# Performance work log

Hardware: AMD Instinct MI355X
Metric: run time of the kernel (lower is better)

Reference implementation:

```python
import jax, jax.numpy as jnp
import numpy as np

B, Q, K, H = 8, 512, 512, 1024
NH, HD = 16, 64
MAX_REL = 512  # max_relative_positions


def setup_inputs() -> dict:
    key = jax.random.key(0)
    ks = jax.random.split(key, 16)
    s = 1.0 / np.sqrt(H)
    inp = {
        "query": jax.random.normal(ks[0], (B, Q, H), jnp.float32),
        "key": jax.random.normal(ks[1], (B, K, H), jnp.float32),
        "value": jax.random.normal(ks[2], (B, K, H), jnp.float32),
        "key_padding_mask": jax.random.randint(ks[3], (B, K), 0, 2, jnp.int32),
        "Wq": jax.random.normal(ks[4], (H, H), jnp.float32) * s,
        "bq": jnp.zeros((H,), jnp.float32),
        "Wk": jax.random.normal(ks[5], (H, H), jnp.float32) * s,
        "bk": jnp.zeros((H,), jnp.float32),
        "Wv": jax.random.normal(ks[6], (H, H), jnp.float32) * s,
        "bv": jnp.zeros((H,), jnp.float32),
        "Wo": jax.random.normal(ks[7], (H, H), jnp.float32) * s,
        "bo": jnp.zeros((H,), jnp.float32),
        "rel_table": jax.random.normal(ks[8], (2 * MAX_REL - 1, NH), jnp.float32) * 0.02,
        "local_bias": jax.random.normal(ks[9], (512, 512), jnp.float32) * 0.1,
        "log_scale": jnp.zeros((1,), jnp.float32),
        "attention_bias": jnp.zeros((1,), jnp.float32),
    }
    return inp


def reference(query, key, value, key_padding_mask, Wq, bq, Wk, bk, Wv, bv, Wo, bo,
              rel_table, local_bias, log_scale, attention_bias):
    # projections -> [B, NH, len, HD]
    q = (query @ Wq + bq).reshape(B, Q, NH, HD).transpose(0, 2, 1, 3)
    k = (key @ Wk + bk).reshape(B, K, NH, HD).transpose(0, 2, 1, 3)
    v = (value @ Wv + bv).reshape(B, K, NH, HD).transpose(0, 2, 1, 3)

    scores = jnp.einsum('bhqd,bhkd->bhqk', q, k) / jnp.sqrt(jnp.float32(HD))

    # relative position bias
    rel = jnp.arange(Q)[:, None] - jnp.arange(K)[None, :]
    bucket = jnp.clip(rel, -(MAX_REL - 1), MAX_REL - 1) + (MAX_REL - 1)
    rel_bias = rel_table[bucket]            # [Q, K, NH]
    scores = scores + rel_bias.transpose(2, 0, 1)[None]  # [1, NH, Q, K]

    # local bias (Q,K <= 512)
    scores = scores + local_bias[:Q, :K][None, None] * 0.05

    scale = jnp.clip(jnp.exp(log_scale), 1.0, 4.0)
    scores = scores * scale + attention_bias

    pad = (key_padding_mask == 0)[:, None, None, :]  # [B,1,1,K]
    scores = jnp.where(pad, -jnp.inf, scores)
    # clamp AFTER masking: -inf -> -50 (padded keys get tiny but nonzero weight)
    scores = jnp.clip(scores, -50.0, 50.0)

    attn = jax.nn.softmax(scores, axis=-1)
    out = jnp.einsum('bhqk,bhkd->bhqd', attn, v)
    out = out.transpose(0, 2, 1, 3).reshape(B, Q, H)
    out = out @ Wo + bo
    return out, attn
```

## Files before the change

### kernel.cpp

```cpp
#include <hip/hip_runtime.h>

#define B_ 8
#define LQ 512
#define LK 512
#define HDIM 1024
#define NH_ 16
#define HD_ 64

typedef unsigned short u16;
typedef __attribute__((ext_vector_type(4))) float f32x4;
typedef __attribute__((ext_vector_type(4))) int i32x4;
typedef __attribute__((ext_vector_type(8))) __bf16 bf16x8;

static __device__ __forceinline__ u16 f2bf(float f) {
    union { float f; unsigned u; } v; v.f = f;
    unsigned u = v.u;
    return (u16)((u + 0x7fffu + ((u >> 16) & 1u)) >> 16);
}

static __device__ __forceinline__ float bf2f(u16 u) {
    union { unsigned u; float f; } v; v.u = ((unsigned)u) << 16;
    return v.f;
}

static __device__ __forceinline__ void gload_lds16(const u16* g, u16* l) {
    __builtin_amdgcn_global_load_lds((const __attribute__((address_space(1))) unsigned*)g,
                                     (__attribute__((address_space(3))) unsigned*)l, 16, 0, 0);
}

__global__ __launch_bounds__(256) void xcast_kernel(
    const float* __restrict__ x0, const float* __restrict__ x1, const float* __restrict__ x2,
    u16* __restrict__ o0, u16* __restrict__ o1, u16* __restrict__ o2)
{
    const float* X; u16* O;
    switch (blockIdx.z) { case 0: X = x0; O = o0; break; case 1: X = x1; O = o1; break;
                          default: X = x2; O = o2; }
    int i = blockIdx.x * 256 + threadIdx.x;
    f32x4 v = ((const f32x4*)X)[i];
    union { u16 u[4]; unsigned long long ull; } p;
    p.u[0] = f2bf(v[0]); p.u[1] = f2bf(v[1]); p.u[2] = f2bf(v[2]); p.u[3] = f2bf(v[3]);
    ((unsigned long long*)O)[i] = p.ull;
}

__global__ void wcast_kernel(const float* __restrict__ w0, const float* __restrict__ w1,
                             const float* __restrict__ w2, const float* __restrict__ w3,
                             u16* __restrict__ o0, u16* __restrict__ o1,
                             u16* __restrict__ o2, u16* __restrict__ o3) {
    const float* W; u16* O;
    switch (blockIdx.z) { case 0: W = w0; O = o0; break; case 1: W = w1; O = o1; break;
                          case 2: W = w2; O = o2; break; default: W = w3; O = o3; }
    __shared__ float t[32][33];
    int tx = threadIdx.x, ty = threadIdx.y;
    int n0 = blockIdx.x * 32, k0 = blockIdx.y * 32;
#pragma unroll
    for (int i = 0; i < 4; i++) {
        int k = ty * 4 + i;
        t[k][tx] = W[(k0 + k) * HDIM + n0 + tx];
    }
    __syncthreads();
#pragma unroll
    for (int i = 0; i < 4; i++) {
        int n = ty * 4 + i;
        O[(n0 + n) * HDIM + k0 + tx] = f2bf(t[tx][n]);
    }
}

__global__ __launch_bounds__(256) void biasprep_kernel(
    const float* __restrict__ rel_table, const float* __restrict__ local_bias,
    const float* __restrict__ log_scale, const float* __restrict__ att_bias,
    u16* __restrict__ Tb)
{
    int idx = blockIdx.x * 256 + threadIdx.x;
    int base = idx * 8;
    int h = base >> 18;
    int rem = base & 262143;
    int qi = rem >> 9, ki0 = rem & 511;
    float scale = fminf(fmaxf(__expf(log_scale[0]), 1.0f), 4.0f);
    float ab = att_bias[0];
    union { u16 u[8]; i32x4 v; } o;
#pragma unroll
    for (int t = 0; t < 8; t++) {
        int ki = ki0 + t;
        float r = rel_table[(qi - ki + 511) * NH_ + h];
        float lb = local_bias[qi * 512 + ki];
        o.u[t] = f2bf((r + lb * 0.05f) * scale + ab);
    }
    *(i32x4*)&Tb[base] = o.v;
}

__global__ __launch_bounds__(256) void proj2_kernel(
    const u16* __restrict__ x0, const u16* __restrict__ x1, const u16* __restrict__ x2,
    const u16* __restrict__ wt0, const u16* __restrict__ wt1, const u16* __restrict__ wt2,
    const float* __restrict__ bi0, const float* __restrict__ bi1, const float* __restrict__ bi2,
    u16* __restrict__ ot0, u16* __restrict__ ot1, u16* __restrict__ ot2)
{
    __shared__ u16 As[128 * 64];
    __shared__ u16 Bs[128 * 64];
    int bid = blockIdx.x;
    int swz = (bid & 7) * 96 + (bid >> 3);
    int z = swz >> 8, rem = swz & 255;
    int Mb = (rem >> 3) * 128, Nb = (rem & 7) * 128;
    const u16* X; const u16* WT; const float* bias; u16* out;
    switch (z) {
        case 0: X = x0; WT = wt0; bias = bi0; out = ot0; break;
        case 1: X = x1; WT = wt1; bias = bi1; out = ot1; break;
        default: X = x2; WT = wt2; bias = bi2; out = ot2; break;
    }
    int tid = threadIdx.x, lane = tid & 63, w = tid >> 6;
    int wm = (w & 1) * 64, wn = (w >> 1) * 64;
    int r16 = lane & 15, kg = lane >> 4;
    int rsw = (r16 & 7) * 8;
    int srow = lane >> 3;
    int scol = 8 * ((lane & 7) ^ (lane >> 3));
    const u16* gA = X + (size_t)Mb * HDIM;
    const u16* gB = WT + (size_t)Nb * HDIM;

    f32x4 acc[4][4] = {};
    for (int k0 = 0; k0 < HDIM; k0 += 64) {
#pragma unroll
        for (int i = 0; i < 4; i++) {
            int c = w * 4 + i;
            int row = c * 8 + srow;
            gload_lds16(&gA[(size_t)row * HDIM + k0 + scol], &As[c * 512]);
            gload_lds16(&gB[(size_t)row * HDIM + k0 + scol], &Bs[c * 512]);
        }
        __syncthreads();
#pragma unroll
        for (int kk = 0; kk < 2; kk++) {
            int colp = (kk * 32 + kg * 8) ^ rsw;
            bf16x8 a[4], b[4];
#pragma unroll
            for (int mt = 0; mt < 4; mt++) a[mt] = *(const bf16x8*)&As[(wm + mt * 16 + r16) * 64 + colp];
#pragma unroll
            for (int nt = 0; nt < 4; nt++) b[nt] = *(const bf16x8*)&Bs[(wn + nt * 16 + r16) * 64 + colp];
#pragma unroll
            for (int mt = 0; mt < 4; mt++)
#pragma unroll
                for (int nt = 0; nt < 4; nt++)
                    acc[mt][nt] = __builtin_amdgcn_mfma_f32_16x16x32_bf16(a[mt], b[nt], acc[mt][nt], 0, 0, 0);
        }
        __syncthreads();
    }
    int cr = (lane >> 4) * 4, cc = lane & 15;
    if (z == 2) {
#pragma unroll
        for (int nt = 0; nt < 4; nt++) {
            int n = Nb + wn + nt * 16 + cc;
            float bv = bias[n];
            int h = n >> 6, d = n & 63;
#pragma unroll
            for (int mt = 0; mt < 4; mt++) {
#pragma unroll
                for (int j = 0; j < 4; j++) {
                    int m = Mb + wm + mt * 16 + cr + j;
                    int b = m >> 9, l = m & 511;
                    out[((size_t)(b * NH_ + h) * HD_ + d) * LK + l] = f2bf(acc[mt][nt][j] + bv);
                }
            }
        }
    } else {
#pragma unroll
        for (int nt = 0; nt < 4; nt++) {
            int n = Nb + wn + nt * 16 + cc;
            float bv = bias[n];
            int h = n >> 6, d = n & 63;
#pragma unroll
            for (int mt = 0; mt < 4; mt++) {
#pragma unroll
                for (int j = 0; j < 4; j++) {
                    int m = Mb + wm + mt * 16 + cr + j;
                    int b = m >> 9, l = m & 511;
                    out[(((b * NH_ + h) * LQ) + l) * HD_ + d] = f2bf(acc[mt][nt][j] + bv);
                }
            }
        }
    }
}

__global__ __launch_bounds__(512) void attn3_kernel(
    const u16* __restrict__ qb, const u16* __restrict__ kb, const u16* __restrict__ vT,
    const int* __restrict__ kpm, const u16* __restrict__ Tb,
    const float* __restrict__ log_scale,
    float* __restrict__ attn_out, u16* __restrict__ ctx)
{
    __shared__ u16 Qs[32][72];
    __shared__ int pmask[512];
    __shared__ float red[32][8];
    __shared__ u16 P[32][516];

    int bh = blockIdx.y;
    int q0 = blockIdx.x * 32;
    int b = bh >> 4, h = bh & 15;
    int tid = threadIdx.x, lane = tid & 63, w = tid >> 6;
    int r16 = lane & 15, kg = lane >> 4;

    float cscale = 0.125f * fminf(fmaxf(__expf(log_scale[0]), 1.0f), 4.0f);

    if (tid < 256) {
        int row = tid >> 3, c8 = tid & 7;
        *(i32x4*)&Qs[row][c8 * 8] = *(const i32x4*)&qb[((size_t)bh * LQ + q0 + row) * HD_ + c8 * 8];
    }
    pmask[tid & 511] = kpm[b * LK + (tid & 511)];
    __syncthreads();

    bf16x8 aq[2][2];
#pragma unroll
    for (int m = 0; m < 2; m++)
#pragma unroll
        for (int kk = 0; kk < 2; kk++)
            aq[m][kk] = *(const bf16x8*)&Qs[m * 16 + r16][kk * 32 + kg * 8];

    f32x4 acc[2][4] = {};
    const u16* kbase = kb + ((size_t)bh * LK + w * 64) * HD_;
#pragma unroll
    for (int nt = 0; nt < 4; nt++) {
        bf16x8 bk0 = *(const bf16x8*)&kbase[(nt * 16 + r16) * HD_ + kg * 8];
        bf16x8 bk1 = *(const bf16x8*)&kbase[(nt * 16 + r16) * HD_ + 32 + kg * 8];
#pragma unroll
        for (int m = 0; m < 2; m++) {
            acc[m][nt] = __builtin_amdgcn_mfma_f32_16x16x32_bf16(aq[m][0], bk0, acc[m][nt], 0, 0, 0);
            acc[m][nt] = __builtin_amdgcn_mfma_f32_16x16x32_bf16(aq[m][1], bk1, acc[m][nt], 0, 0, 0);
        }
    }

    const u16* Th = Tb + ((size_t)h << 18);
    float ps[2][4] = {};
#pragma unroll
    for (int m = 0; m < 2; m++) {
#pragma unroll
        for (int nt = 0; nt < 4; nt++) {
            int ki = w * 64 + nt * 16 + r16;
            bool masked = (pmask[ki] == 0);
#pragma unroll
            for (int j = 0; j < 4; j++) {
                int row = m * 16 + kg * 4 + j;
                int qi = q0 + row;
                float s = fmaf(acc[m][nt][j], cscale, bf2f(Th[qi * 512 + ki]));
                s = fminf(fmaxf(s, -50.0f), 50.0f);
                s = masked ? -50.0f : s;
                float e = __expf(s - 50.0f);
                acc[m][nt][j] = e;
                ps[m][j] += e;
                P[row][w * 64 + nt * 16 + r16] = f2bf(e);
            }
        }
    }
#pragma unroll
    for (int m = 0; m < 2; m++)
#pragma unroll
        for (int j = 0; j < 4; j++) {
            float v = ps[m][j];
            v += __shfl_xor(v, 1);
            v += __shfl_xor(v, 2);
            v += __shfl_xor(v, 4);
            v += __shfl_xor(v, 8);
            ps[m][j] = v;
        }
    if (r16 == 0) {
#pragma unroll
        for (int m = 0; m < 2; m++)
#pragma unroll
            for (int j = 0; j < 4; j++) red[m * 16 + kg * 4 + j][w] = ps[m][j];
    }
    __syncthreads();

    float inv[2][4];
#pragma unroll
    for (int m = 0; m < 2; m++)
#pragma unroll
        for (int j = 0; j < 4; j++) {
            int row = m * 16 + kg * 4 + j;
            f32x4 s0 = *(const f32x4*)&red[row][0];
            f32x4 s1 = *(const f32x4*)&red[row][4];
            float sum = (s0[0] + s0[1]) + (s0[2] + s0[3]) + (s1[0] + s1[1]) + (s1[2] + s1[3]);
            inv[m][j] = __builtin_amdgcn_rcpf(sum);
        }

    float* dst = attn_out + ((size_t)bh * LQ + q0) * (size_t)LK + w * 64;
#pragma unroll
    for (int m = 0; m < 2; m++)
#pragma unroll
        for (int j = 0; j < 4; j++) {
            int row = m * 16 + kg * 4 + j;
#pragma unroll
            for (int nt = 0; nt < 4; nt++)
                __builtin_nontemporal_store(acc[m][nt][j] * inv[m][j],
                                            &dst[(size_t)row * LK + nt * 16 + r16]);
        }

    int qh = w & 1, dt = w >> 1;
    const u16* vbase = vT + ((size_t)bh * HD_ + dt * 16 + r16) * LK;
    f32x4 po = {};
#pragma unroll
    for (int kt = 0; kt < 16; kt++) {
        bf16x8 af = *(const bf16x8*)&P[qh * 16 + r16][kt * 32 + kg * 8];
        bf16x8 bvf = *(const bf16x8*)&vbase[kt * 32 + kg * 8];
        po = __builtin_amdgcn_mfma_f32_16x16x32_bf16(af, bvf, po, 0, 0, 0);
    }
#pragma unroll
    for (int j = 0; j < 4; j++) {
        int q = q0 + qh * 16 + kg * 4 + j;
        ctx[((size_t)(b * LQ + q)) * HDIM + h * HD_ + dt * 16 + r16] = f2bf(po[j] * inv[qh][j]);
    }
}

__global__ __launch_bounds__(256) void oproj2_kernel(
    const u16* __restrict__ ctx, const u16* __restrict__ WT,
    const float* __restrict__ bias, float* __restrict__ out)
{
    __shared__ u16 As[128 * 64];
    __shared__ u16 Bs[128 * 64];
    int bid = blockIdx.x;
    int idx = (bid & 7) * 32 + (bid >> 3);
    int Mb = (idx >> 3) * 128, Nb = (idx & 7) * 128;
    int tid = threadIdx.x, lane = tid & 63, w = tid >> 6;
    int wm = (w & 1) * 64, wn = (w >> 1) * 64;
    int r16 = lane & 15, kg = lane >> 4;
    int rsw = (r16 & 7) * 8;
    int srow = lane >> 3;
    int scol = 8 * ((lane & 7) ^ (lane >> 3));
    const u16* gA = ctx + (size_t)Mb * HDIM;
    const u16* gB = WT + (size_t)Nb * HDIM;

    f32x4 acc[4][4] = {};
    for (int k0 = 0; k0 < HDIM; k0 += 64) {
#pragma unroll
        for (int i = 0; i < 4; i++) {
            int c = w * 4 + i;
            int row = c * 8 + srow;
            gload_lds16(&gA[(size_t)row * HDIM + k0 + scol], &As[c * 512]);
            gload_lds16(&gB[(size_t)row * HDIM + k0 + scol], &Bs[c * 512]);
        }
        __syncthreads();
#pragma unroll
        for (int kk = 0; kk < 2; kk++) {
            int colp = (kk * 32 + kg * 8) ^ rsw;
            bf16x8 a[4], b[4];
#pragma unroll
            for (int mt = 0; mt < 4; mt++) a[mt] = *(const bf16x8*)&As[(wm + mt * 16 + r16) * 64 + colp];
#pragma unroll
            for (int nt = 0; nt < 4; nt++) b[nt] = *(const bf16x8*)&Bs[(wn + nt * 16 + r16) * 64 + colp];
#pragma unroll
            for (int mt = 0; mt < 4; mt++)
#pragma unroll
                for (int nt = 0; nt < 4; nt++)
                    acc[mt][nt] = __builtin_amdgcn_mfma_f32_16x16x32_bf16(a[mt], b[nt], acc[mt][nt], 0, 0, 0);
        }
        __syncthreads();
    }
    int cr = (lane >> 4) * 4, cc = lane & 15;
#pragma unroll
    for (int nt = 0; nt < 4; nt++) {
        int n = Nb + wn + nt * 16 + cc;
        float bv = bias[n];
#pragma unroll
        for (int mt = 0; mt < 4; mt++) {
#pragma unroll
            for (int j = 0; j < 4; j++) {
                int m = Mb + wm + mt * 16 + cr + j;
                out[(size_t)m * HDIM + n] = acc[mt][nt][j] + bv;
            }
        }
    }
}

extern "C" void kernel_launch(void* const* d_in, const int* in_sizes, int n_in,
                              void* d_out, int out_size, void* d_ws, size_t ws_size,
                              hipStream_t stream) {
    (void)in_sizes; (void)n_in; (void)out_size; (void)ws_size;
    const float* query = (const float*)d_in[0];
    const float* key_  = (const float*)d_in[1];
    const float* value = (const float*)d_in[2];
    const int*   kpm   = (const int*)d_in[3];
    const float* Wq = (const float*)d_in[4];  const float* bq = (const float*)d_in[5];
    const float* Wk = (const float*)d_in[6];  const float* bk = (const float*)d_in[7];
    const float* Wv = (const float*)d_in[8];  const float* bv = (const float*)d_in[9];
    const float* Wo = (const float*)d_in[10]; const float* bo = (const float*)d_in[11];
    const float* rel_table  = (const float*)d_in[12];
    const float* local_bias = (const float*)d_in[13];
    const float* log_scale  = (const float*)d_in[14];
    const float* att_bias   = (const float*)d_in[15];

    char* ws = (char*)d_ws;
    u16* WTq = (u16*)(ws + 0ull);
    u16* WTk = (u16*)(ws + (2ull << 20));
    u16* WTv = (u16*)(ws + (4ull << 20));
    u16* WTo = (u16*)(ws + (6ull << 20));
    u16* qb  = (u16*)(ws + (8ull << 20));
    u16* kb  = (u16*)(ws + (16ull << 20));
    u16* vT  = (u16*)(ws + (24ull << 20));
    u16* xq  = (u16*)(ws + (32ull << 20));
    u16* ctx = (u16*)(ws + (40ull << 20));
    u16* xk  = (u16*)(ws + (40ull << 20));
    u16* xv  = (u16*)(ws + (48ull << 20));
    u16* Tb  = (u16*)(ws + (48ull << 20));

    float* out  = (float*)d_out;
    float* attn = out + (size_t)4096 * 1024;

    xcast_kernel<<<dim3(4096, 1, 3), 256, 0, stream>>>(query, key_, value, xq, xk, xv);
    wcast_kernel<<<dim3(32, 32, 4), dim3(32, 8), 0, stream>>>(Wq, Wk, Wv, Wo, WTq, WTk, WTv, WTo);
    proj2_kernel<<<768, 256, 0, stream>>>(xq, xk, xv, WTq, WTk, WTv, bq, bk, bv, qb, kb, vT);
    biasprep_kernel<<<2048, 256, 0, stream>>>(rel_table, local_bias, log_scale, att_bias, Tb);
    attn3_kernel<<<dim3(16, 128), 512, 0, stream>>>(qb, kb, vT, kpm, Tb, log_scale, attn, ctx);
    oproj2_kernel<<<256, 256, 0, stream>>>(ctx, WTo, bo, out);
}
```

Before: 182.1 us.

## Transpose bias table, add separate V transpose, and coalesce attention-probability stores

The bias table is now laid out key-major, so the attention kernel reads four query biases with one 8-byte load. The V projection is written in normal layout and transposed by a new tiled kernel instead of scattered stores in the GEMM epilogue. The fp32 attention-probability output is written from LDS as contiguous vectorized rows instead of strided per-lane nontemporal stores. The kernel also swizzles the block order, sets an occupancy hint, and splits PV accumulation into two chains. The cost is an extra launch and pass over V, plus probabilities written from their bf16-rounded values.

```diff
diff --git a/kernel.cpp b/kernel.cpp
--- a/kernel.cpp
+++ b/kernel.cpp
@@ -74,13 +74,13 @@
     int base = idx * 8;
     int h = base >> 18;
     int rem = base & 262143;
-    int qi = rem >> 9, ki0 = rem & 511;
+    int ki = rem >> 9, qi0 = rem & 511;
     float scale = fminf(fmaxf(__expf(log_scale[0]), 1.0f), 4.0f);
     float ab = att_bias[0];
     union { u16 u[8]; i32x4 v; } o;
 #pragma unroll
     for (int t = 0; t < 8; t++) {
-        int ki = ki0 + t;
+        int qi = qi0 + t;
         float r = rel_table[(qi - ki + 511) * NH_ + h];
         float lb = local_bias[qi * 512 + ki];
         o.u[t] = f2bf((r + lb * 0.05f) * scale + ab);
@@ -142,42 +142,44 @@
         __syncthreads();
     }
     int cr = (lane >> 4) * 4, cc = lane & 15;
-    if (z == 2) {
-#pragma unroll
-        for (int nt = 0; nt < 4; nt++) {
-            int n = Nb + wn + nt * 16 + cc;
-            float bv = bias[n];
-            int h = n >> 6, d = n & 63;
-#pragma unroll
-            for (int mt = 0; mt < 4; mt++) {
-#pragma unroll
-                for (int j = 0; j < 4; j++) {
-                    int m = Mb + wm + mt * 16 + cr + j;
-                    int b = m >> 9, l = m & 511;
-                    out[((size_t)(b * NH_ + h) * HD_ + d) * LK + l] = f2bf(acc[mt][nt][j] + bv);
-                }
+#pragma unroll
+    for (int nt = 0; nt < 4; nt++) {
+        int n = Nb + wn + nt * 16 + cc;
+        float bv = bias[n];
+        int h = n >> 6, d = n & 63;
+#pragma unroll
+        for (int mt = 0; mt < 4; mt++) {
+#pragma unroll
+            for (int j = 0; j < 4; j++) {
+                int m = Mb + wm + mt * 16 + cr + j;
+                int b = m >> 9, l = m & 511;
+                out[(((b * NH_ + h) * LQ) + l) * HD_ + d] = f2bf(acc[mt][nt][j] + bv);
             }
         }
-    } else {
-#pragma unroll
-        for (int nt = 0; nt < 4; nt++) {
-            int n = Nb + wn + nt * 16 + cc;
-            float bv = bias[n];
-            int h = n >> 6, d = n & 63;
-#pragma unroll
-            for (int mt = 0; mt < 4; mt++) {
-#pragma unroll
-                for (int j = 0; j < 4; j++) {
-                    int m = Mb + wm + mt * 16 + cr + j;
-                    int b = m >> 9, l = m & 511;
-                    out[(((b * NH_ + h) * LQ) + l) * HD_ + d] = f2bf(acc[mt][nt][j] + bv);
-                }
-            }
-        }
-    }
-}
-
-__global__ __launch_bounds__(512) void attn3_kernel(
+    }
+}
+
+__global__ void vtrans_kernel(const u16* __restrict__ vb, u16* __restrict__ vT) {
+    int bh = blockIdx.z;
+    int k0 = blockIdx.x * 32, d0 = blockIdx.y * 32;
+    __shared__ u16 t[32][33];
+    int tx = threadIdx.x, ty = threadIdx.y;
+    const u16* src = vb + (size_t)bh * (LK * HD_);
+    u16* dst = vT + (size_t)bh * (LK * HD_);
+#pragma unroll
+    for (int i = 0; i < 4; i++) {
+        int k = ty * 4 + i;
+        t[k][tx] = src[(k0 + k) * HD_ + d0 + tx];
+    }
+    __syncthreads();
+#pragma unroll
+    for (int i = 0; i < 4; i++) {
+        int d = ty * 4 + i;
+        dst[(d0 + d) * LK + k0 + tx] = t[tx][d];
+    }
+}
+
+__global__ __launch_bounds__(512, 8) void attn4_kernel(
     const u16* __restrict__ qb, const u16* __restrict__ kb, const u16* __restrict__ vT,
     const int* __restrict__ kpm, const u16* __restrict__ Tb,
     const float* __restrict__ log_scale,
@@ -186,10 +188,13 @@
     __shared__ u16 Qs[32][72];
     __shared__ int pmask[512];
     __shared__ float red[32][8];
+    __shared__ float sinv[32];
     __shared__ u16 P[32][516];
 
-    int bh = blockIdx.y;
-    int q0 = blockIdx.x * 32;
+    int bid = blockIdx.x;
+    int swz = (bid & 7) * 256 + (bid >> 3);
+    int bh = swz >> 4;
+    int q0 = (swz & 15) * 32;
     int b = bh >> 4, h = bh & 15;
     int tid = threadIdx.x, lane = tid & 63, w = tid >> 6;
     int r16 = lane & 15, kg = lane >> 4;
@@ -231,15 +236,15 @@
         for (int nt = 0; nt < 4; nt++) {
             int ki = w * 64 + nt * 16 + r16;
             bool masked = (pmask[ki] == 0);
+            union { u16 u[4]; unsigned long long ull; } tv;
+            tv.ull = *(const unsigned long long*)&Th[(size_t)ki * 512 + q0 + m * 16 + kg * 4];
 #pragma unroll
             for (int j = 0; j < 4; j++) {
                 int row = m * 16 + kg * 4 + j;
-                int qi = q0 + row;
-                float s = fmaf(acc[m][nt][j], cscale, bf2f(Th[qi * 512 + ki]));
+                float s = fmaf(acc[m][nt][j], cscale, bf2f(tv.u[j]));
                 s = fminf(fmaxf(s, -50.0f), 50.0f);
                 s = masked ? -50.0f : s;
                 float e = __expf(s - 50.0f);
-                acc[m][nt][j] = e;
                 ps[m][j] += e;
                 P[row][w * 64 + nt * 16 + r16] = f2bf(e);
             }
@@ -264,43 +269,51 @@
     }
     __syncthreads();
 
-    float inv[2][4];
-#pragma unroll
-    for (int m = 0; m < 2; m++)
-#pragma unroll
-        for (int j = 0; j < 4; j++) {
-            int row = m * 16 + kg * 4 + j;
-            f32x4 s0 = *(const f32x4*)&red[row][0];
-            f32x4 s1 = *(const f32x4*)&red[row][4];
-            float sum = (s0[0] + s0[1]) + (s0[2] + s0[3]) + (s1[0] + s1[1]) + (s1[2] + s1[3]);
-            inv[m][j] = __builtin_amdgcn_rcpf(sum);
-        }
-
-    float* dst = attn_out + ((size_t)bh * LQ + q0) * (size_t)LK + w * 64;
-#pragma unroll
-    for (int m = 0; m < 2; m++)
-#pragma unroll
-        for (int j = 0; j < 4; j++) {
-            int row = m * 16 + kg * 4 + j;
-#pragma unroll
-            for (int nt = 0; nt < 4; nt++)
-                __builtin_nontemporal_store(acc[m][nt][j] * inv[m][j],
-                                            &dst[(size_t)row * LK + nt * 16 + r16]);
-        }
+    if (tid < 32) {
+        float s = 0.f;
+#pragma unroll
+        for (int ww = 0; ww < 8; ww++) s += red[tid][ww];
+        sinv[tid] = __builtin_amdgcn_rcpf(s);
+    }
+    __syncthreads();
+
+    {
+        float* dst = attn_out + ((size_t)bh * LQ + q0) * (size_t)LK;
+#pragma unroll
+        for (int i = 0; i < 4; i++) {
+            int g = tid + i * 512;
+            int row = g >> 6, c8 = (g & 63) * 8;
+            float iv = sinv[row];
+            bf16x8 pv8 = *(const bf16x8*)&P[row][c8];
+            f32x4 o0, o1;
+#pragma unroll
+            for (int t = 0; t < 4; t++) {
+                o0[t] = bf2f(((const u16*)&pv8)[t]) * iv;
+                o1[t] = bf2f(((const u16*)&pv8)[4 + t]) * iv;
+            }
+            *(f32x4*)&dst[(size_t)row * LK + c8] = o0;
+            *(f32x4*)&dst[(size_t)row * LK + c8 + 4] = o1;
+        }
+    }
 
     int qh = w & 1, dt = w >> 1;
     const u16* vbase = vT + ((size_t)bh * HD_ + dt * 16 + r16) * LK;
-    f32x4 po = {};
-#pragma unroll
-    for (int kt = 0; kt < 16; kt++) {
-        bf16x8 af = *(const bf16x8*)&P[qh * 16 + r16][kt * 32 + kg * 8];
-        bf16x8 bvf = *(const bf16x8*)&vbase[kt * 32 + kg * 8];
-        po = __builtin_amdgcn_mfma_f32_16x16x32_bf16(af, bvf, po, 0, 0, 0);
+    f32x4 poa = {}, pob = {};
+#pragma unroll
+    for (int kt = 0; kt < 8; kt++) {
+        bf16x8 afa = *(const bf16x8*)&P[qh * 16 + r16][kt * 64 + kg * 8];
+        bf16x8 bva = *(const bf16x8*)&vbase[kt * 64 + kg * 8];
+        poa = __builtin_amdgcn_mfma_f32_16x16x32_bf16(afa, bva, poa, 0, 0, 0);
+        bf16x8 afb = *(const bf16x8*)&P[qh * 16 + r16][kt * 64 + 32 + kg * 8];
+        bf16x8 bvb = *(const bf16x8*)&vbase[kt * 64 + 32 + kg * 8];
+        pob = __builtin_amdgcn_mfma_f32_16x16x32_bf16(afb, bvb, pob, 0, 0, 0);
     }
 #pragma unroll
     for (int j = 0; j < 4; j++) {
-        int q = q0 + qh * 16 + kg * 4 + j;
-        ctx[((size_t)(b * LQ + q)) * HDIM + h * HD_ + dt * 16 + r16] = f2bf(po[j] * inv[qh][j]);
+        int rloc = qh * 16 + kg * 4 + j;
+        int q = q0 + rloc;
+        float v = (poa[j] + pob[j]) * sinv[rloc];
+        ctx[((size_t)(b * LQ + q)) * HDIM + h * HD_ + dt * 16 + r16] = f2bf(v);
     }
 }
 
@@ -388,10 +401,11 @@
     u16* WTo = (u16*)(ws + (6ull << 20));
     u16* qb  = (u16*)(ws + (8ull << 20));
     u16* kb  = (u16*)(ws + (16ull << 20));
-    u16* vT  = (u16*)(ws + (24ull << 20));
+    u16* vb  = (u16*)(ws + (24ull << 20));
     u16* xq  = (u16*)(ws + (32ull << 20));
+    u16* vT  = (u16*)(ws + (32ull << 20));
+    u16* xk  = (u16*)(ws + (40ull << 20));
     u16* ctx = (u16*)(ws + (40ull << 20));
-    u16* xk  = (u16*)(ws + (40ull << 20));
     u16* xv  = (u16*)(ws + (48ull << 20));
     u16* Tb  = (u16*)(ws + (48ull << 20));
 
@@ -400,8 +414,9 @@
 
     xcast_kernel<<<dim3(4096, 1, 3), 256, 0, stream>>>(query, key_, value, xq, xk, xv);
     wcast_kernel<<<dim3(32, 32, 4), dim3(32, 8), 0, stream>>>(Wq, Wk, Wv, Wo, WTq, WTk, WTv, WTo);
-    proj2_kernel<<<768, 256, 0, stream>>>(xq, xk, xv, WTq, WTk, WTv, bq, bk, bv, qb, kb, vT);
+    proj2_kernel<<<768, 256, 0, stream>>>(xq, xk, xv, WTq, WTk, WTv, bq, bk, bv, qb, kb, vb);
+    vtrans_kernel<<<dim3(16, 2, 128), dim3(32, 8), 0, stream>>>(vb, vT);
     biasprep_kernel<<<2048, 256, 0, stream>>>(rel_table, local_bias, log_scale, att_bias, Tb);
-    attn3_kernel<<<dim3(16, 128), 512, 0, stream>>>(qb, kb, vT, kpm, Tb, log_scale, attn, ctx);
+    attn4_kernel<<<2048, 512, 0, stream>>>(qb, kb, vT, kpm, Tb, log_scale, attn, ctx);
     oproj2_kernel<<<256, 256, 0, stream>>>(ctx, WTo, bo, out);
 }
```

New measurement: 187.4 us. +2.9%, slower.
